# Performance work log

Hardware: AMD Instinct MI355X
Metric: run time of the kernel (lower is better)

## Reference

```python
import jax, jax.numpy as jnp
import numpy as np

E, T, D_IN, D_OUT = 8, 2048, 2048, 1408


def setup_inputs() -> dict:
    key = jax.random.key(0)
    k_x, k_g, k_d, k_u = jax.random.split(key, 4)
    std = 0.02
    return {
        "x": jax.random.normal(k_x, (E, T, D_IN), dtype=jnp.float32),
        "gate_proj": jax.random.normal(k_g, (E, D_IN, D_OUT), dtype=jnp.float32) * std,
        "down_proj": jax.random.normal(k_d, (E, D_IN, D_OUT), dtype=jnp.float32) * std,
        "up_proj": jax.random.normal(k_u, (E, D_OUT, D_IN), dtype=jnp.float32) * std,
    }


def reference(x, gate_proj, down_proj, up_proj):
    # Grouped-expert SwiGLU: h = silu(x @ W_gate) * (x @ W_down); out = h @ W_up
    # x: [E, T, d_in]; gate/down: [E, d_in, d_out]; up: [E, d_out, d_in]
    g = jnp.einsum('etd,edh->eth', x, gate_proj)
    u = jnp.einsum('etd,edh->eth', x, down_proj)
    h = jax.nn.silu(g) * u                      # [E, T, d_out]
    out = jnp.einsum('eth,ehd->etd', h, up_proj)  # [E, T, d_in]
    return out
```

## Files before the change

### kernel.cpp

```cpp
#include <hip/hip_runtime.h>
#include <stdint.h>
#include <stddef.h>

#define NE    8
#define NT    2048
#define NDIN  2048
#define NDOUT 1408

typedef __bf16 bf16;
typedef __attribute__((ext_vector_type(8))) __bf16 bf16x8;
typedef __attribute__((ext_vector_type(4))) float f32x4;

static_assert(NDOUT % 128 == 0 && NDIN % 128 == 0 && NT % 128 == 0, "tile divisibility");

__device__ __forceinline__ void gl_lds16(const void* g, void* lds) {
  __builtin_amdgcn_global_load_lds(
      (const __attribute__((address_space(1))) void*)g,
      (__attribute__((address_space(3))) void*)lds,
      16, 0, 0);
}

__global__ void k_cvt_x(const float* __restrict__ x, bf16* __restrict__ xb) {
  const long n4 = (long)NE * NT * NDIN / 4;
  long i = (long)blockIdx.x * blockDim.x + threadIdx.x;
  const long stride = (long)gridDim.x * blockDim.x;
  for (; i < n4; i += stride) {
    float4 v = ((const float4*)x)[i];
    union { bf16 b[4]; uint64_t u; } p;
    p.b[0] = (bf16)v.x; p.b[1] = (bf16)v.y; p.b[2] = (bf16)v.z; p.b[3] = (bf16)v.w;
    ((uint64_t*)xb)[i] = p.u;
  }
}

__global__ void k_transpose(const float* __restrict__ W, bf16* __restrict__ Wt,
                            int K, int N) {
  __shared__ bf16 tile[32][34];
  const size_t mat = (size_t)K * N;
  const float* Wp = W + blockIdx.z * mat;
  bf16* Wtp = Wt + blockIdx.z * mat;
  const int n0 = blockIdx.x * 32, k0 = blockIdx.y * 32;
  const int tx = threadIdx.x & 31, ty = threadIdx.x >> 5;
#pragma unroll
  for (int i = 0; i < 4; i++) {
    int k = ty + i * 8;
    tile[k][tx] = (bf16)Wp[(size_t)(k0 + k) * N + n0 + tx];
  }
  __syncthreads();
#pragma unroll
  for (int i = 0; i < 4; i++) {
    int n = ty + i * 8;
    Wtp[(size_t)(n0 + n) * K + k0 + tx] = tile[tx][n];
  }
}

#define BM 128
#define BN 128
#define BK 32

__global__ __launch_bounds__(256, 2) void k_gemm_swiglu(
    const bf16* __restrict__ xb,
    const bf16* __restrict__ gt,
    const bf16* __restrict__ dt,
    bf16* __restrict__ h) {
  __shared__ __align__(16) bf16 As[BM * BK];
  __shared__ __align__(16) bf16 Bgs[BN * BK];
  __shared__ __align__(16) bf16 Bds[BN * BK];

  const int e = blockIdx.z;
  const int m0 = blockIdx.y * BM;
  const int n0 = blockIdx.x * BN;

  const bf16* Ap  = xb + ((size_t)e * NT + m0) * NDIN;
  const bf16* Bgp = gt + ((size_t)e * NDOUT + n0) * NDIN;
  const bf16* Bdp = dt + ((size_t)e * NDOUT + n0) * NDIN;

  const int lane = threadIdx.x & 63;
  const int wave = threadIdx.x >> 6;
  const int wm = wave >> 1, wn = wave & 1;

  const int lrow = lane >> 2;
  const int lk   = (lane & 3) * 8;
  const int fr = lane & 15;
  const int fk = (lane >> 4) * 8;

  f32x4 accg[4][4], accu[4][4];
#pragma unroll
  for (int i = 0; i < 4; i++)
#pragma unroll
    for (int j = 0; j < 4; j++) {
      accg[i][j] = f32x4{0.f, 0.f, 0.f, 0.f};
      accu[i][j] = f32x4{0.f, 0.f, 0.f, 0.f};
    }

  for (int k0 = 0; k0 < NDIN; k0 += BK) {
#pragma unroll
    for (int i = 0; i < 2; i++) {
      const int r = wave * 32 + i * 16;
      const size_t go = (size_t)(r + lrow) * NDIN + k0 + lk;
      gl_lds16(Ap + go,  As  + r * BK);
      gl_lds16(Bgp + go, Bgs + r * BK);
      gl_lds16(Bdp + go, Bds + r * BK);
    }
    __syncthreads();

    bf16x8 af[4], bg[4], bd[4];
#pragma unroll
    for (int t = 0; t < 4; t++) {
      af[t] = *(const bf16x8*)(As  + (wm * 64 + t * 16 + fr) * BK + fk);
      bg[t] = *(const bf16x8*)(Bgs + (wn * 64 + t * 16 + fr) * BK + fk);
      bd[t] = *(const bf16x8*)(Bds + (wn * 64 + t * 16 + fr) * BK + fk);
    }
#pragma unroll
    for (int mt = 0; mt < 4; mt++)
#pragma unroll
      for (int nt = 0; nt < 4; nt++) {
        accg[mt][nt] = __builtin_amdgcn_mfma_f32_16x16x32_bf16(af[mt], bg[nt], accg[mt][nt], 0, 0, 0);
        accu[mt][nt] = __builtin_amdgcn_mfma_f32_16x16x32_bf16(af[mt], bd[nt], accu[mt][nt], 0, 0, 0);
      }
    __syncthreads();
  }

  bf16* hp = h + ((size_t)e * NT + m0) * NDOUT + n0;
  const int cc = lane & 15;
  const int cr = (lane >> 4) * 4;
#pragma unroll
  for (int mt = 0; mt < 4; mt++)
#pragma unroll
    for (int nt = 0; nt < 4; nt++) {
      f32x4 g4 = accg[mt][nt], u4 = accu[mt][nt];
#pragma unroll
      for (int r = 0; r < 4; r++) {
        float gg = g4[r];
        float s = gg / (1.f + __expf(-gg));
        float hh = s * u4[r];
        hp[(size_t)(wm * 64 + mt * 16 + cr + r) * NDOUT + wn * 64 + nt * 16 + cc] = (bf16)hh;
      }
    }
}

__global__ __launch_bounds__(256, 2) void k_gemm_out(
    const bf16* __restrict__ hb,
    const bf16* __restrict__ ut,
    float* __restrict__ out) {
  __shared__ __align__(16) bf16 As[BM * BK];
  __shared__ __align__(16) bf16 Bs[BN * BK];

  const int e = blockIdx.z;
  const int m0 = blockIdx.y * BM;
  const int n0 = blockIdx.x * BN;

  const bf16* Ap = hb + ((size_t)e * NT + m0) * NDOUT;
  const bf16* Bp = ut + ((size_t)e * NDIN + n0) * NDOUT;

  const int lane = threadIdx.x & 63;
  const int wave = threadIdx.x >> 6;
  const int wm = wave >> 1, wn = wave & 1;
  const int lrow = lane >> 2;
  const int lk   = (lane & 3) * 8;
  const int fr = lane & 15;
  const int fk = (lane >> 4) * 8;

  f32x4 acc[4][4];
#pragma unroll
  for (int i = 0; i < 4; i++)
#pragma unroll
    for (int j = 0; j < 4; j++) acc[i][j] = f32x4{0.f, 0.f, 0.f, 0.f};

  for (int k0 = 0; k0 < NDOUT; k0 += BK) {
#pragma unroll
    for (int i = 0; i < 2; i++) {
      const int r = wave * 32 + i * 16;
      const size_t go = (size_t)(r + lrow) * NDOUT + k0 + lk;
      gl_lds16(Ap + go, As + r * BK);
      gl_lds16(Bp + go, Bs + r * BK);
    }
    __syncthreads();

    bf16x8 af[4], bfr[4];
#pragma unroll
    for (int t = 0; t < 4; t++) {
      af[t]  = *(const bf16x8*)(As + (wm * 64 + t * 16 + fr) * BK + fk);
      bfr[t] = *(const bf16x8*)(Bs + (wn * 64 + t * 16 + fr) * BK + fk);
    }
#pragma unroll
    for (int mt = 0; mt < 4; mt++)
#pragma unroll
      for (int nt = 0; nt < 4; nt++)
        acc[mt][nt] = __builtin_amdgcn_mfma_f32_16x16x32_bf16(af[mt], bfr[nt], acc[mt][nt], 0, 0, 0);
    __syncthreads();
  }

  float* op = out + ((size_t)e * NT + m0) * NDIN + n0;
  const int cc = lane & 15;
  const int cr = (lane >> 4) * 4;
#pragma unroll
  for (int mt = 0; mt < 4; mt++)
#pragma unroll
    for (int nt = 0; nt < 4; nt++) {
#pragma unroll
      for (int r = 0; r < 4; r++)
        op[(size_t)(wm * 64 + mt * 16 + cr + r) * NDIN + wn * 64 + nt * 16 + cc] =
            acc[mt][nt][r];
    }
}

extern "C" void kernel_launch(void* const* d_in, const int* in_sizes, int n_in,
                              void* d_out, int out_size, void* d_ws, size_t ws_size,
                              hipStream_t stream) {
  const float* x    = (const float*)d_in[0];
  const float* gate = (const float*)d_in[1];
  const float* down = (const float*)d_in[2];
  const float* up   = (const float*)d_in[3];

  bf16* xb = (bf16*)d_out;

  const size_t WE = (size_t)NE * NDOUT * NDIN;
  bf16* gate_t = (bf16*)d_ws;
  bf16* down_t = gate_t + WE;
  bf16* up_t   = down_t + WE;
  bf16* hbuf   = up_t + WE;

  k_cvt_x<<<2048, 256, 0, stream>>>(x, xb);
  k_transpose<<<dim3(NDOUT / 32, NDIN / 32, NE), 256, 0, stream>>>(gate, gate_t, NDIN, NDOUT);
  k_transpose<<<dim3(NDOUT / 32, NDIN / 32, NE), 256, 0, stream>>>(down, down_t, NDIN, NDOUT);
  k_transpose<<<dim3(NDIN / 32, NDOUT / 32, NE), 256, 0, stream>>>(up, up_t, NDOUT, NDIN);

  k_gemm_swiglu<<<dim3(NDOUT / BN, NT / BM, NE), 256, 0, stream>>>(xb, gate_t, down_t, hbuf);
  k_gemm_out<<<dim3(NDIN / BN, NT / BM, NE), 256, 0, stream>>>(hbuf, up_t, (float*)d_out);
}
```

Baseline: 790.9 us.

## Vectorize weight transpose stores and interleave experts in GEMM grid order

The transpose kernel now uses a 128x32 tile, so each thread writes 16-byte bf16x8 vectors along K instead of scalar 2-byte stores. This is meant to cut the cost of the weight preprocessing passes. Both GEMMs switch to a flattened 1D grid with the expert index in the low bits, so consecutive blocks go to different experts. The likely aim is to spread work across XCDs/L2 partitions per expert, at some cost to tile locality within an expert.

```diff
diff --git a/kernel.cpp b/kernel.cpp
--- a/kernel.cpp
+++ b/kernel.cpp
@@ -11,7 +11,16 @@
 typedef __attribute__((ext_vector_type(8))) __bf16 bf16x8;
 typedef __attribute__((ext_vector_type(4))) float f32x4;
 
+#define BM 128
+#define BN 128
+#define BK 32
+
+#define NTM   (NT / BM)
+#define NTN1  (NDOUT / BN)
+#define NTN2  (NDIN / BN)
+
 static_assert(NDOUT % 128 == 0 && NDIN % 128 == 0 && NT % 128 == 0, "tile divisibility");
+static_assert(NDOUT % 32 == 0 && NDIN % 32 == 0, "transpose divisibility");
 
 __device__ __forceinline__ void gl_lds16(const void* g, void* lds) {
   __builtin_amdgcn_global_load_lds(
@@ -34,28 +43,28 @@
 
 __global__ void k_transpose(const float* __restrict__ W, bf16* __restrict__ Wt,
                             int K, int N) {
-  __shared__ bf16 tile[32][34];
+  __shared__ bf16 tile[128][34];
   const size_t mat = (size_t)K * N;
   const float* Wp = W + blockIdx.z * mat;
   bf16* Wtp = Wt + blockIdx.z * mat;
-  const int n0 = blockIdx.x * 32, k0 = blockIdx.y * 32;
-  const int tx = threadIdx.x & 31, ty = threadIdx.x >> 5;
-#pragma unroll
-  for (int i = 0; i < 4; i++) {
-    int k = ty + i * 8;
-    tile[k][tx] = (bf16)Wp[(size_t)(k0 + k) * N + n0 + tx];
+  const int n0 = blockIdx.x * 32, k0 = blockIdx.y * 128;
+  const int tn = threadIdx.x & 31, tk = threadIdx.x >> 5;
+#pragma unroll
+  for (int i = 0; i < 16; i++) {
+    int k = tk + i * 8;
+    tile[k][tn] = (bf16)Wp[(size_t)(k0 + k) * N + n0 + tn];
   }
   __syncthreads();
-#pragma unroll
-  for (int i = 0; i < 4; i++) {
-    int n = ty + i * 8;
-    Wtp[(size_t)(n0 + n) * K + k0 + tx] = tile[tx][n];
-  }
-}
-
-#define BM 128
-#define BN 128
-#define BK 32
+  const int wn = threadIdx.x >> 4, wkk = (threadIdx.x & 15) * 8;
+#pragma unroll
+  for (int i = 0; i < 2; i++) {
+    int n = wn + i * 16;
+    union { bf16 b[8]; bf16x8 v; } p;
+#pragma unroll
+    for (int j = 0; j < 8; j++) p.b[j] = tile[wkk + j][n];
+    *(bf16x8*)(Wtp + (size_t)(n0 + n) * K + k0 + wkk) = p.v;
+  }
+}
 
 __global__ __launch_bounds__(256, 2) void k_gemm_swiglu(
     const bf16* __restrict__ xb,
@@ -66,9 +75,11 @@
   __shared__ __align__(16) bf16 Bgs[BN * BK];
   __shared__ __align__(16) bf16 Bds[BN * BK];
 
-  const int e = blockIdx.z;
-  const int m0 = blockIdx.y * BM;
-  const int n0 = blockIdx.x * BN;
+  const int lin = blockIdx.x;
+  const int e = lin & 7;
+  const int idx = lin >> 3;
+  const int m0 = (idx / NTN1) * BM;
+  const int n0 = (idx % NTN1) * BN;
 
   const bf16* Ap  = xb + ((size_t)e * NT + m0) * NDIN;
   const bf16* Bgp = gt + ((size_t)e * NDOUT + n0) * NDIN;
@@ -145,9 +156,11 @@
   __shared__ __align__(16) bf16 As[BM * BK];
   __shared__ __align__(16) bf16 Bs[BN * BK];
 
-  const int e = blockIdx.z;
-  const int m0 = blockIdx.y * BM;
-  const int n0 = blockIdx.x * BN;
+  const int lin = blockIdx.x;
+  const int e = lin & 7;
+  const int idx = lin >> 3;
+  const int m0 = (idx / NTN2) * BM;
+  const int n0 = (idx % NTN2) * BN;
 
   const bf16* Ap = hb + ((size_t)e * NT + m0) * NDOUT;
   const bf16* Bp = ut + ((size_t)e * NDIN + n0) * NDOUT;
@@ -221,10 +234,10 @@
   bf16* hbuf   = up_t + WE;
 
   k_cvt_x<<<2048, 256, 0, stream>>>(x, xb);
-  k_transpose<<<dim3(NDOUT / 32, NDIN / 32, NE), 256, 0, stream>>>(gate, gate_t, NDIN, NDOUT);
-  k_transpose<<<dim3(NDOUT / 32, NDIN / 32, NE), 256, 0, stream>>>(down, down_t, NDIN, NDOUT);
-  k_transpose<<<dim3(NDIN / 32, NDOUT / 32, NE), 256, 0, stream>>>(up, up_t, NDOUT, NDIN);
-
-  k_gemm_swiglu<<<dim3(NDOUT / BN, NT / BM, NE), 256, 0, stream>>>(xb, gate_t, down_t, hbuf);
-  k_gemm_out<<<dim3(NDIN / BN, NT / BM, NE), 256, 0, stream>>>(hbuf, up_t, (float*)d_out);
-}
+  k_transpose<<<dim3(NDOUT / 32, NDIN / 128, NE), 256, 0, stream>>>(gate, gate_t, NDIN, NDOUT);
+  k_transpose<<<dim3(NDOUT / 32, NDIN / 128, NE), 256, 0, stream>>>(down, down_t, NDIN, NDOUT);
+  k_transpose<<<dim3(NDIN / 32, NDOUT / 128, NE), 256, 0, stream>>>(up, up_t, NDOUT, NDIN);
+
+  k_gemm_swiglu<<<NTM * NTN1 * NE, 256, 0, stream>>>(xb, gate_t, down_t, hbuf);
+  k_gemm_out<<<NTM * NTN2 * NE, 256, 0, stream>>>(hbuf, up_t, (float*)d_out);
+}
```

New measurement: 758.3 us. 1.04x faster.
